# Performance work log

Hardware: AMD Instinct MI355X
Metric: run time of the kernel (lower is better)

Reference implementation:

```python
import jax, jax.numpy as jnp
import numpy as np

H = 1024
V = 50257


def setup_inputs() -> dict:
    key = jax.random.key(0)
    ks = jax.random.split(key, 10)
    s = 0.02
    return {
        "x": jax.random.randint(ks[0], (1,), 0, V, dtype=jnp.int32),
        "h0": jax.random.normal(ks[1], (1, 1, H), jnp.float32),
        "c0": jax.random.normal(ks[2], (1, 1, H), jnp.float32),
        "emb": jax.random.normal(ks[3], (V, H), jnp.float32) * s,
        "w_ih": jax.random.normal(ks[4], (4 * H, H), jnp.float32) * s,
        "w_hh": jax.random.normal(ks[5], (4 * H, H), jnp.float32) * s,
        "b_ih": jax.random.normal(ks[6], (4 * H,), jnp.float32) * s,
        "b_hh": jax.random.normal(ks[7], (4 * H,), jnp.float32) * s,
        "w_out": jax.random.normal(ks[8], (V, H), jnp.float32) * s,
        "b_out": jax.random.normal(ks[9], (V,), jnp.float32) * s,
    }


def reference(x, h0, c0, emb, w_ih, w_hh, b_ih, b_hh, w_out, b_out):
    # embedding lookup + view(1,1,-1) + relu -> [1, H]
    e = jax.nn.relu(emb[x].reshape(1, H))
    h = h0[0]  # [1, H]
    c = c0[0]  # [1, H]
    # single LSTM cell step; PyTorch gate order: i, f, g, o
    gates = e @ w_ih.T + b_ih + h @ w_hh.T + b_hh  # [1, 4H]
    i, f, g, o = jnp.split(gates, 4, axis=1)
    c_new = jax.nn.sigmoid(f) * c + jax.nn.sigmoid(i) * jnp.tanh(g)
    h_new = jax.nn.sigmoid(o) * jnp.tanh(c_new)
    # output projection + log-softmax over vocab
    logits = h_new @ w_out.T + b_out  # [1, V]
    out = jax.nn.log_softmax(logits, axis=1)
    return out, (h_new[None, :, :], c_new[None, :, :])
```

## Files before the change

### kernel.cpp

```cpp
#include <hip/hip_runtime.h>
#include <math.h>

#define HH 1024
#define VV 50257
#define NLB 2048
#define NWAVE (NLB * 4)
#define NTAIL (VV - 6 * NWAVE)

__device__ __forceinline__ float wave_allreduce_sum(float v) {
#pragma unroll
    for (int off = 1; off < 64; off <<= 1) v += __shfl_xor(v, off, 64);
    return v;
}

__device__ __forceinline__ void lse_comb(float& m, float& s, float om, float os) {
    float M = fmaxf(m, om);
    s = s * __expf(m - M) + os * __expf(om - M);
    m = M;
}

__device__ __forceinline__ float sigmoidf(float x) { return 1.0f / (1.0f + __expf(-x)); }

__device__ __forceinline__ float dot4(float4 a, float4 b) {
    return a.x * b.x + a.y * b.y + a.z * b.z + a.w * b.w;
}

__global__ __launch_bounds__(512, 8) void k_gatecell(
    const int* __restrict__ x, const float* __restrict__ emb,
    const float* __restrict__ h0, const float* __restrict__ c0,
    const float* __restrict__ w_ih, const float* __restrict__ w_hh,
    const float* __restrict__ b_ih, const float* __restrict__ b_hh,
    float* __restrict__ out) {
    __shared__ float sg2[8];
    const int j = blockIdx.x;
    const int w = threadIdx.x >> 6;
    const int lane = threadIdx.x & 63;
    const int g = w >> 1, hf = w & 1;
    const int row = g * HH + j;
    const int base = hf * 512 + lane * 8;

    const float* e  = emb + (size_t)x[0] * HH + base;
    const float* wi = w_ih + (size_t)row * HH + base;
    const float* wh = w_hh + (size_t)row * HH + base;
    const float* hp = h0 + base;

    float4 wi0 = *reinterpret_cast<const float4*>(wi);
    float4 wi1 = *reinterpret_cast<const float4*>(wi + 4);
    float4 wh0 = *reinterpret_cast<const float4*>(wh);
    float4 wh1 = *reinterpret_cast<const float4*>(wh + 4);
    float4 e0  = *reinterpret_cast<const float4*>(e);
    float4 e1  = *reinterpret_cast<const float4*>(e + 4);
    float4 hv0 = *reinterpret_cast<const float4*>(hp);
    float4 hv1 = *reinterpret_cast<const float4*>(hp + 4);
    e0.x = fmaxf(e0.x, 0.f); e0.y = fmaxf(e0.y, 0.f);
    e0.z = fmaxf(e0.z, 0.f); e0.w = fmaxf(e0.w, 0.f);
    e1.x = fmaxf(e1.x, 0.f); e1.y = fmaxf(e1.y, 0.f);
    e1.z = fmaxf(e1.z, 0.f); e1.w = fmaxf(e1.w, 0.f);

    float acc = dot4(wi0, e0) + dot4(wi1, e1) + dot4(wh0, hv0) + dot4(wh1, hv1);
    acc = wave_allreduce_sum(acc);
    if (lane == 0)
        sg2[w] = acc + (hf == 0 ? b_ih[row] + b_hh[row] : 0.0f);
    __syncthreads();
    if (threadIdx.x == 0) {
        float ig = sigmoidf(sg2[0] + sg2[1]);
        float fg = sigmoidf(sg2[2] + sg2[3]);
        float gg = tanhf(sg2[4] + sg2[5]);
        float og = sigmoidf(sg2[6] + sg2[7]);
        float c = fg * c0[j] + ig * gg;
        float h = og * tanhf(c);
        out[VV + j] = h;
        out[VV + HH + j] = c;
    }
}

__global__ __launch_bounds__(256, 8) void k_logits_lse(
    const float* __restrict__ w_out, const float* __restrict__ b_out,
    const float* __restrict__ h, float* __restrict__ logits,
    float* __restrict__ pm, float* __restrict__ ps) {
    __shared__ float sm[4], ss[4];
    const int w = threadIdx.x >> 6;
    const int lane = threadIdx.x & 63;
    const int wid = blockIdx.x * 4 + w;
    const bool has7 = (wid < NTAIL);

    const float* hp = h + lane * 4;
    float4 h0v = *reinterpret_cast<const float4*>(hp);
    float4 h1v = *reinterpret_cast<const float4*>(hp + 256);
    float4 h2v = *reinterpret_cast<const float4*>(hp + 512);
    float4 h3v = *reinterpret_cast<const float4*>(hp + 768);

    const float* wb = w_out + (size_t)wid * HH + lane * 4;
    float m = -1e30f, s = 0.0f;

    float4 n0 = *reinterpret_cast<const float4*>(wb);
    float4 n1 = *reinterpret_cast<const float4*>(wb + 256);
    float4 n2 = *reinterpret_cast<const float4*>(wb + 512);
    float4 n3 = *reinterpret_cast<const float4*>(wb + 768);

#pragma unroll
    for (int c = 0; c < 6; ++c) {
        float4 a0 = n0, a1 = n1, a2 = n2, a3 = n3;
        if (c < 5 || has7) {
            const float* pn = wb + (size_t)(c + 1) * NWAVE * HH;
            n0 = *reinterpret_cast<const float4*>(pn);
            n1 = *reinterpret_cast<const float4*>(pn + 256);
            n2 = *reinterpret_cast<const float4*>(pn + 512);
            n3 = *reinterpret_cast<const float4*>(pn + 768);
        }
        float acc = dot4(a0, h0v) + dot4(a1, h1v) + dot4(a2, h2v) + dot4(a3, h3v);
        acc = wave_allreduce_sum(acc);
        int row = wid + c * NWAVE;
        float v = acc + b_out[row];
        if (lane == 0) logits[row] = v;
        float M = fmaxf(m, v);
        s = s * __expf(m - M) + __expf(v - M);
        m = M;
    }
    if (has7) {
        float acc = dot4(n0, h0v) + dot4(n1, h1v) + dot4(n2, h2v) + dot4(n3, h3v);
        acc = wave_allreduce_sum(acc);
        int row = wid + 6 * NWAVE;
        float v = acc + b_out[row];
        if (lane == 0) logits[row] = v;
        float M = fmaxf(m, v);
        s = s * __expf(m - M) + __expf(v - M);
        m = M;
    }

    if (lane == 0) { sm[w] = m; ss[w] = s; }
    __syncthreads();
    if (threadIdx.x == 0) {
        float M = sm[0], S = ss[0];
#pragma unroll
        for (int q = 1; q < 4; ++q) lse_comb(M, S, sm[q], ss[q]);
        pm[blockIdx.x] = M;
        ps[blockIdx.x] = S;
    }
}

__global__ __launch_bounds__(256) void k_final(
    const float* __restrict__ logits, const float* __restrict__ pm,
    const float* __restrict__ ps, float* __restrict__ out) {
    __shared__ float sm[4], ss[4];
    __shared__ float sZ;
    int tid = threadIdx.x;
    int lane = tid & 63;
    float m = -1e30f, s = 0.0f;
    for (int p = tid; p < NLB; p += 256) {
        lse_comb(m, s, pm[p], ps[p]);
    }
#pragma unroll
    for (int off = 1; off < 64; off <<= 1) {
        float om = __shfl_xor(m, off, 64);
        float os = __shfl_xor(s, off, 64);
        lse_comb(m, s, om, os);
    }
    if (lane == 0) { sm[tid >> 6] = m; ss[tid >> 6] = s; }
    __syncthreads();
    if (tid == 0) {
        float M = sm[0], S = ss[0];
#pragma unroll
        for (int q = 1; q < 4; ++q) lse_comb(M, S, sm[q], ss[q]);
        sZ = M + logf(S);
    }
    __syncthreads();
    float Z = sZ;
    for (int i = blockIdx.x * 256 + tid; i < VV; i += gridDim.x * 256)
        out[i] = logits[i] - Z;
}

extern "C" void kernel_launch(void* const* d_in, const int* in_sizes, int n_in,
                              void* d_out, int out_size, void* d_ws, size_t ws_size,
                              hipStream_t stream) {
    const int*   x     = (const int*)d_in[0];
    const float* h0    = (const float*)d_in[1];
    const float* c0    = (const float*)d_in[2];
    const float* emb   = (const float*)d_in[3];
    const float* w_ih  = (const float*)d_in[4];
    const float* w_hh  = (const float*)d_in[5];
    const float* b_ih  = (const float*)d_in[6];
    const float* b_hh  = (const float*)d_in[7];
    const float* w_out = (const float*)d_in[8];
    const float* b_out = (const float*)d_in[9];
    float* out = (float*)d_out;
    float* ws  = (float*)d_ws;

    float* logits = ws;
    float* pm     = ws + 50304;
    float* ps     = pm + NLB;

    k_gatecell<<<HH, 512, 0, stream>>>(x, emb, h0, c0, w_ih, w_hh, b_ih, b_hh, out);
    k_logits_lse<<<NLB, 256, 0, stream>>>(w_out, b_out, out + VV, logits, pm, ps);
    k_final<<<256, 256, 0, stream>>>(logits, pm, ps, out);
}
```

Before: 52.11 us.

## Give each wave a contiguous row range with deeper prefetch and shared h

```diff
diff --git a/kernel.cpp b/kernel.cpp
--- a/kernel.cpp
+++ b/kernel.cpp
@@ -3,15 +3,8 @@
 
 #define HH 1024
 #define VV 50257
-#define NLB 2048
-#define NWAVE (NLB * 4)
-#define NTAIL (VV - 6 * NWAVE)
-
-__device__ __forceinline__ float wave_allreduce_sum(float v) {
-#pragma unroll
-    for (int off = 1; off < 64; off <<= 1) v += __shfl_xor(v, off, 64);
-    return v;
-}
+#define NLB 1024
+#define NEXTRA 1105
 
 __device__ __forceinline__ void lse_comb(float& m, float& s, float om, float os) {
     float M = fmaxf(m, om);
@@ -25,7 +18,7 @@
     return a.x * b.x + a.y * b.y + a.z * b.z + a.w * b.w;
 }
 
-__global__ __launch_bounds__(512, 8) void k_gatecell(
+__global__ __launch_bounds__(512) void k_gatecell(
     const int* __restrict__ x, const float* __restrict__ emb,
     const float* __restrict__ h0, const float* __restrict__ c0,
     const float* __restrict__ w_ih, const float* __restrict__ w_hh,
@@ -58,7 +51,8 @@
     e1.z = fmaxf(e1.z, 0.f); e1.w = fmaxf(e1.w, 0.f);
 
     float acc = dot4(wi0, e0) + dot4(wi1, e1) + dot4(wh0, hv0) + dot4(wh1, hv1);
-    acc = wave_allreduce_sum(acc);
+#pragma unroll
+    for (int off = 1; off < 64; off <<= 1) acc += __shfl_xor(acc, off, 64);
     if (lane == 0)
         sg2[w] = acc + (hf == 0 ? b_ih[row] + b_hh[row] : 0.0f);
     __syncthreads();
@@ -74,63 +68,102 @@
     }
 }
 
-__global__ __launch_bounds__(256, 8) void k_logits_lse(
+__global__ __launch_bounds__(256, 4) void k_logits_lse(
     const float* __restrict__ w_out, const float* __restrict__ b_out,
     const float* __restrict__ h, float* __restrict__ logits,
     float* __restrict__ pm, float* __restrict__ ps) {
+    __shared__ float4 hs[256];
     __shared__ float sm[4], ss[4];
-    const int w = threadIdx.x >> 6;
-    const int lane = threadIdx.x & 63;
+    const int tid = threadIdx.x;
+    const int w = tid >> 6;
+    const int lane = tid & 63;
+
+    hs[tid] = reinterpret_cast<const float4*>(h)[tid];
+    __syncthreads();
+
     const int wid = blockIdx.x * 4 + w;
-    const bool has7 = (wid < NTAIL);
-
-    const float* hp = h + lane * 4;
-    float4 h0v = *reinterpret_cast<const float4*>(hp);
-    float4 h1v = *reinterpret_cast<const float4*>(hp + 256);
-    float4 h2v = *reinterpret_cast<const float4*>(hp + 512);
-    float4 h3v = *reinterpret_cast<const float4*>(hp + 768);
-
-    const float* wb = w_out + (size_t)wid * HH + lane * 4;
+    const bool extra = (wid < NEXTRA);
+    const int base = wid * 12 + (extra ? wid : NEXTRA);
+    const float* wp = w_out + (size_t)base * HH + lane * 4;
+
+    float4 A[3][4], B[3][4], T[4];
+
+#pragma unroll
+    for (int p = 0; p < 2; ++p) {
+        const float* pa = wp + (size_t)(2 * p) * HH;
+        const float* pb = pa + HH;
+#pragma unroll
+        for (int c = 0; c < 4; ++c) {
+            A[p][c] = *reinterpret_cast<const float4*>(pa + c * 256);
+            B[p][c] = *reinterpret_cast<const float4*>(pb + c * 256);
+        }
+    }
+
     float m = -1e30f, s = 0.0f;
-
-    float4 n0 = *reinterpret_cast<const float4*>(wb);
-    float4 n1 = *reinterpret_cast<const float4*>(wb + 256);
-    float4 n2 = *reinterpret_cast<const float4*>(wb + 512);
-    float4 n3 = *reinterpret_cast<const float4*>(wb + 768);
-
-#pragma unroll
-    for (int c = 0; c < 6; ++c) {
-        float4 a0 = n0, a1 = n1, a2 = n2, a3 = n3;
-        if (c < 5 || has7) {
-            const float* pn = wb + (size_t)(c + 1) * NWAVE * HH;
-            n0 = *reinterpret_cast<const float4*>(pn);
-            n1 = *reinterpret_cast<const float4*>(pn + 256);
-            n2 = *reinterpret_cast<const float4*>(pn + 512);
-            n3 = *reinterpret_cast<const float4*>(pn + 768);
-        }
-        float acc = dot4(a0, h0v) + dot4(a1, h1v) + dot4(a2, h2v) + dot4(a3, h3v);
-        acc = wave_allreduce_sum(acc);
-        int row = wid + c * NWAVE;
-        float v = acc + b_out[row];
-        if (lane == 0) logits[row] = v;
+#pragma unroll
+    for (int k = 0; k < 6; ++k) {
+        if (k < 4) {
+            const int sl = (k + 2) % 3;
+            const float* pa = wp + (size_t)(2 * (k + 2)) * HH;
+            const float* pb = pa + HH;
+#pragma unroll
+            for (int c = 0; c < 4; ++c) {
+                A[sl][c] = *reinterpret_cast<const float4*>(pa + c * 256);
+                B[sl][c] = *reinterpret_cast<const float4*>(pb + c * 256);
+            }
+        } else if (k == 4 && extra) {
+            const float* pt = wp + (size_t)12 * HH;
+#pragma unroll
+            for (int c = 0; c < 4; ++c)
+                T[c] = *reinterpret_cast<const float4*>(pt + c * 256);
+        }
+        const int cs = k % 3;
+        float accA = 0.0f, accB = 0.0f;
+#pragma unroll
+        for (int c = 0; c < 4; ++c) {
+            float4 hc = hs[lane + c * 64];
+            accA += dot4(A[cs][c], hc);
+            accB += dot4(B[cs][c], hc);
+        }
+#pragma unroll
+        for (int off = 1; off < 64; off <<= 1) {
+            accA += __shfl_xor(accA, off, 64);
+            accB += __shfl_xor(accB, off, 64);
+        }
+        const int rA = base + 2 * k;
+        const float vA = accA + b_out[rA];
+        const float vB = accB + b_out[rA + 1];
+        if (lane == 0) {
+            logits[rA] = vA;
+            logits[rA + 1] = vB;
+        }
+        float M = fmaxf(m, vA);
+        s = s * __expf(m - M) + __expf(vA - M);
+        m = M;
+        M = fmaxf(m, vB);
+        s = s * __expf(m - M) + __expf(vB - M);
+        m = M;
+    }
+    if (extra) {
+        float acc = 0.0f;
+#pragma unroll
+        for (int c = 0; c < 4; ++c) {
+            float4 hc = hs[lane + c * 64];
+            acc += dot4(T[c], hc);
+        }
+#pragma unroll
+        for (int off = 1; off < 64; off <<= 1) acc += __shfl_xor(acc, off, 64);
+        const int r = base + 12;
+        const float v = acc + b_out[r];
+        if (lane == 0) logits[r] = v;
         float M = fmaxf(m, v);
         s = s * __expf(m - M) + __expf(v - M);
         m = M;
     }
-    if (has7) {
-        float acc = dot4(n0, h0v) + dot4(n1, h1v) + dot4(n2, h2v) + dot4(n3, h3v);
-        acc = wave_allreduce_sum(acc);
-        int row = wid + 6 * NWAVE;
-        float v = acc + b_out[row];
-        if (lane == 0) logits[row] = v;
-        float M = fmaxf(m, v);
-        s = s * __expf(m - M) + __expf(v - M);
-        m = M;
-    }
 
     if (lane == 0) { sm[w] = m; ss[w] = s; }
     __syncthreads();
-    if (threadIdx.x == 0) {
+    if (tid == 0) {
         float M = sm[0], S = ss[0];
 #pragma unroll
         for (int q = 1; q < 4; ++q) lse_comb(M, S, sm[q], ss[q]);
@@ -147,7 +180,9 @@
     int tid = threadIdx.x;
     int lane = tid & 63;
     float m = -1e30f, s = 0.0f;
-    for (int p = tid; p < NLB; p += 256) {
+#pragma unroll
+    for (int t = 0; t < NLB / 256; ++t) {
+        int p = tid + t * 256;
         lse_comb(m, s, pm[p], ps[p]);
     }
 #pragma unroll
```

Measured after the change: 50.40 us. 1.03x faster.
